# Optimization experiments

Hardware: AMD Instinct MI355X
Metric: run time of the kernel (lower is better)

## Reference

```python
import jax, jax.numpy as jnp
import numpy as np
from jax import lax

RADIUS = 8
EPS = 1e-3
EPS_LOG = 1e-6
EPS_SCALE = 1e-4
A_COMP = 0.7
B_SHIFT = 0.0
DETAIL_GAIN = 1.0
DOWN = 0.5
# detail_threshold=0 and target_mean=0 -> those branches are inactive (defaults)

DN = (('NCHW', 'OIHW', 'NCHW'))


def _box_filter(x4d):
    """Separable box filter on [1,1,H,W] with reflect padding, kernel 2r+1."""
    k = 2 * RADIUS + 1
    xp = jnp.pad(x4d, ((0, 0), (0, 0), (RADIUS, RADIUS), (RADIUS, RADIUS)), mode='reflect')
    kh = jnp.full((1, 1, 1, k), 1.0 / k, dtype=x4d.dtype)
    kv = jnp.full((1, 1, k, 1), 1.0 / k, dtype=x4d.dtype)
    y = lax.conv_general_dilated(xp, kh, (1, 1), 'VALID', dimension_numbers=DN)
    y = lax.conv_general_dilated(y, kv, (1, 1), 'VALID', dimension_numbers=DN)
    return y


def _guided_filter(img):
    """Self-guided filter on a 2D image [H, W]."""
    x4 = img[None, None]
    mean_I = _box_filter(x4)
    mean_II = _box_filter(x4 * x4)
    var_I = mean_II - mean_I * mean_I
    a = var_I / (var_I + EPS)
    b = mean_I - a * mean_I
    out = _box_filter(a) * x4 + _box_filter(b)
    return out[0, 0]


def _bilinear_resize(img, oh, ow):
    """Bilinear resize [H,W] -> [oh,ow], half-pixel centers (align_corners=False),
    no antialias, matching torch F.interpolate(mode='bilinear')."""
    H, W = img.shape
    ys = jnp.maximum((jnp.arange(oh, dtype=img.dtype) + 0.5) * (H / oh) - 0.5, 0.0)
    xs = jnp.maximum((jnp.arange(ow, dtype=img.dtype) + 0.5) * (W / ow) - 0.5, 0.0)
    y0 = jnp.floor(ys)
    x0 = jnp.floor(xs)
    wy = (ys - y0)[:, None]
    wx = (xs - x0)[None, :]
    y0i = jnp.clip(y0.astype(jnp.int32), 0, H - 1)
    y1i = jnp.minimum(y0i + 1, H - 1)
    x0i = jnp.clip(x0.astype(jnp.int32), 0, W - 1)
    x1i = jnp.minimum(x0i + 1, W - 1)
    # vertical lerp, then horizontal lerp (separable)
    vert = img[y0i, :] * (1.0 - wy) + img[y1i, :] * wy       # [oh, W]
    out = vert[:, x0i] * (1.0 - wx) + vert[:, x1i] * wx      # [oh, ow]
    return out


def setup_inputs() -> dict:
    key = jax.random.key(0)
    x = jax.random.uniform(key, (2160, 3840, 3), dtype=jnp.float32)
    return {"x": x}


def reference(x) -> jnp.ndarray:
    H, W = x.shape[0], x.shape[1]
    Y = 0.2126 * x[..., 0] + 0.7152 * x[..., 1] + 0.0722 * x[..., 2]
    Y_log = jnp.log2(jnp.maximum(Y, EPS_LOG))
    # fast path: downsample -> guided filter -> upsample
    dh, dw = int(H * DOWN), int(W * DOWN)
    Y_log_down = _bilinear_resize(Y_log, dh, dw)
    Y_base_down = _guided_filter(Y_log_down)
    Y_base = _bilinear_resize(Y_base_down, H, W)
    Y_detail = Y_log - Y_base  # detail_threshold=0 -> no suppression
    Y_tm = (A_COMP * Y_base + B_SHIFT) + DETAIL_GAIN * Y_detail
    Y_out = jnp.exp2(Y_tm)
    scale = Y_out / (Y + EPS_SCALE)
    out = jnp.clip(x * scale[..., None], 0.0, 1.0)
    # target_mean=0 -> no global mean rescale
    return out
```

## Files before the change

### kernel.cpp

```cpp
#include <hip/hip_runtime.h>
#include <math.h>

#define H_FULL 2160
#define W_FULL 3840
#define H_D    1080
#define W_D    1920
#define KLEN   17
#define INV_K2 (1.0f/289.0f)

typedef float f32x4 __attribute__((ext_vector_type(4)));

#if __has_builtin(__builtin_amdgcn_logf)
#define FAST_LOG2(x) __builtin_amdgcn_logf(x)
#else
#define FAST_LOG2(x) log2f(x)
#endif
#if __has_builtin(__builtin_amdgcn_exp2f)
#define FAST_EXP2(x) __builtin_amdgcn_exp2f(x)
#else
#define FAST_EXP2(x) exp2f(x)
#endif
#if __has_builtin(__builtin_amdgcn_rcpf)
#define FAST_RCP(x) __builtin_amdgcn_rcpf(x)
#else
#define FAST_RCP(x) (1.0f/(x))
#endif

static __device__ __forceinline__ int refl(int i, int n) {
    if (i < 0) i = -i;
    else if (i >= n) i = 2*n - 2 - i;
    return i;
}
static __device__ __forceinline__ float lum(float r, float g, float b) {
    return 0.2126f*r + 0.7152f*g + 0.0722f*b;
}
static __device__ __forceinline__ float lg(float y) {
    return FAST_LOG2(fmaxf(y, 1e-6f));
}
static __device__ __forceinline__ void nt_store4(float* p, float a, float b,
                                                 float c, float d) {
    f32x4 v; v.x = a; v.y = b; v.z = c; v.w = d;
    __builtin_nontemporal_store(v, (f32x4*)p);
}

__global__ __launch_bounds__(256) void k_down(const float* __restrict__ x,
                                              float* __restrict__ I) {
    int t = blockIdx.x * 256 + threadIdx.x;
    int p = t * 2;
    int i = p / W_D;
    int j = p - i * W_D;
    const float4* r0 = (const float4*)(x + ((size_t)(2*i)   * W_FULL + 2*j) * 3);
    const float4* r1 = (const float4*)(x + ((size_t)(2*i+1) * W_FULL + 2*j) * 3);
    float4 a0 = r0[0], a1 = r0[1], a2 = r0[2];
    float4 b0 = r1[0], b1 = r1[1], b2 = r1[2];
    float y00 = lum(a0.x,a0.y,a0.z), y01 = lum(a0.w,a1.x,a1.y);
    float y02 = lum(a1.z,a1.w,a2.x), y03 = lum(a2.y,a2.z,a2.w);
    float y10 = lum(b0.x,b0.y,b0.z), y11 = lum(b0.w,b1.x,b1.y);
    float y12 = lum(b1.z,b1.w,b2.x), y13 = lum(b2.y,b2.z,b2.w);
    float o0 = 0.25f * (lg(y00)+lg(y01)+lg(y10)+lg(y11));
    float o1 = 0.25f * (lg(y02)+lg(y03)+lg(y12)+lg(y13));
    *(float2*)(I + (size_t)i * W_D + j) = make_float2(o0, o1);
}

__global__ __launch_bounds__(512, 6) void k_fused5(const float* __restrict__ I,
                                                   const float* __restrict__ x,
                                                   float* __restrict__ out) {
    __shared__ char lds[52088];
    float*  sIc   = (float*) (lds);
    float*  sIf   = (float*) (lds + 4760);
    float2* ab    = (float2*)(lds + 4760);
    float2* hI    = (float2*)(lds + 25160);
    float2* hab   = (float2*)(lds + 25160);
    float*  baseL = (float*) (lds + 39160);
    float*  stage = (float*) (lds + 8192);

    int tx0 = blockIdx.x * 32;
    int ty0 = blockIdx.y * 32;
    int tid = threadIdx.x;

    for (int e = tid; e < 66 * 66; e += 512) {
        int r = e / 66, c = e - r * 66;
        sIf[r * 67 + c] =
            I[(size_t)refl(ty0 - 17 + r, H_D) * W_D + refl(tx0 - 17 + c, W_D)];
    }
    __syncthreads();

    if (tid < 330) {
        int r = tid / 5, run = tid - (tid / 5) * 5;
        int c0 = run * 10;
        const float* p = &sIf[r * 67 + c0];
        float s1 = 0.f, s2 = 0.f;
        #pragma unroll
        for (int k = 0; k < KLEN; ++k) { float v = p[k]; s1 += v; s2 += v * v; }
        float2* o = &hI[r * 51 + c0];
        o[0] = make_float2(s1, s2);
        #pragma unroll
        for (int m = 1; m < 10; ++m) {
            float vo = p[m - 1], vi = p[m + 16];
            s1 += vi - vo;
            s2 += vi * vi - vo * vo;
            o[m] = make_float2(s1, s2);
        }
    }
    for (int e = tid; e < 34 * 34; e += 512) {
        int r = e / 34, c = e - r * 34;
        sIc[r * 35 + c] = sIf[(r + 16) * 67 + (c + 16)];
    }
    __syncthreads();

    if (tid < 250) {
        int c = tid % 50, run = tid / 50;
        int r0 = run * 10;
        const float2* p = &hI[r0 * 51 + c];
        float s1 = 0.f, s2 = 0.f;
        #pragma unroll
        for (int k = 0; k < KLEN; ++k) { float2 v = p[k * 51]; s1 += v.x; s2 += v.y; }
        float2* o = &ab[r0 * 51 + c];
        #pragma unroll
        for (int m = 0; m < 10; ++m) {
            if (m) {
                float2 vi = p[(m + 16) * 51], vo = p[(m - 1) * 51];
                s1 += vi.x - vo.x;
                s2 += vi.y - vo.y;
            }
            float mI  = s1 * INV_K2;
            float mII = s2 * INV_K2;
            float var = mII - mI * mI;
            float av  = var / (var + 1e-3f);
            o[m * 51] = make_float2(av, mI - av * mI);
        }
    }
    __syncthreads();

    if (tid < 200) {
        int r = tid % 50, run = tid / 50;
        int c0  = (run < 2) ? run * 9 : 18 + (run - 2) * 8;
        int len = (run < 2) ? 9 : 8;
        const float2* p = &ab[r * 51 + c0];
        float sa = 0.f, sb = 0.f;
        #pragma unroll
        for (int k = 0; k < KLEN; ++k) { float2 v = p[k]; sa += v.x; sb += v.y; }
        float2* o = &hab[r * 35 + c0];
        o[0] = make_float2(sa, sb);
        #pragma unroll
        for (int m = 1; m < 9; ++m) {
            if (m < len) {
                float2 vi = p[m + 16], vo = p[m - 1];
                sa += vi.x - vo.x;
                sb += vi.y - vo.y;
                o[m] = make_float2(sa, sb);
            }
        }
    }
    __syncthreads();

    if (tid < 136) {
        int cc = tid % 34, run = tid / 34;
        int r0  = (run < 2) ? run * 9 : 18 + (run - 2) * 8;
        int len = (run < 2) ? 9 : 8;
        const float2* p = &hab[r0 * 35 + cc];
        float sa = 0.f, sb = 0.f;
        #pragma unroll
        for (int k = 0; k < KLEN; ++k) { float2 v = p[k * 35]; sa += v.x; sb += v.y; }
        #pragma unroll
        for (int m = 0; m < 9; ++m) {
            if (m < len) {
                if (m) {
                    float2 vi = p[(m + 16) * 35], vo = p[(m - 1) * 35];
                    sa += vi.x - vo.x;
                    sb += vi.y - vo.y;
                }
                int br = r0 + m;
                baseL[br * 35 + cc] =
                    (sa * INV_K2) * sIc[br * 35 + cc] + sb * INV_K2;
            }
        }
    }
    __syncthreads();

    int q  = tid & 15;
    int r  = tid >> 4;
    int gc0 = tx0 + 2 * q - 1;
    int l0 = max(gc0, 0) - (tx0 - 1);
    int l1 = 2 * q + 1, l2 = 2 * q + 2;
    int l3 = min(gc0 + 3, W_D - 1) - (tx0 - 1);
    int j0 = tx0 * 2 + q * 4;

    #pragma unroll
    for (int s = 0; s < 2; ++s) {
        int oy = ty0 * 2 + r + s * 32;
        if (oy < H_FULL) {
            int y0g = (oy - 1) >> 1;
            int ly0 = max(y0g, 0) - (ty0 - 1);
            int ly1 = min(y0g + 1, H_D - 1) - (ty0 - 1);
            float wy = (oy & 1) ? 0.25f : 0.75f;
            const float* b0r = &baseL[ly0 * 35];
            const float* b1r = &baseL[ly1 * 35];
            float v0 = b0r[l0] + (b1r[l0] - b0r[l0]) * wy;
            float v1 = b0r[l1] + (b1r[l1] - b0r[l1]) * wy;
            float v2 = b0r[l2] + (b1r[l2] - b0r[l2]) * wy;
            float v3 = b0r[l3] + (b1r[l3] - b0r[l3]) * wy;
            float Yb[4];
            Yb[0] = v0 + (v1 - v0) * 0.75f;
            Yb[1] = v1 + (v2 - v1) * 0.25f;
            Yb[2] = v1 + (v2 - v1) * 0.75f;
            Yb[3] = v2 + (v3 - v2) * 0.25f;

            size_t off = ((size_t)oy * W_FULL + j0) * 3;
            const float4* px = (const float4*)(x + off);
            float4 q0 = px[0], q1 = px[1], q2 = px[2];
            float rgb[12] = {q0.x,q0.y,q0.z,q0.w, q1.x,q1.y,q1.z,q1.w, q2.x,q2.y,q2.z,q2.w};
            float res[12];
            #pragma unroll
            for (int k = 0; k < 4; ++k) {
                float rr = rgb[3*k], gg = rgb[3*k+1], bb = rgb[3*k+2];
                float Y = lum(rr, gg, bb);
                float sc = fmaxf(Y, 1e-6f) * FAST_EXP2(-0.3f * Yb[k]) * FAST_RCP(Y + 1e-4f);
                res[3*k]   = fminf(fmaxf(rr * sc, 0.f), 1.f);
                res[3*k+1] = fminf(fmaxf(gg * sc, 0.f), 1.f);
                res[3*k+2] = fminf(fmaxf(bb * sc, 0.f), 1.f);
            }
            float* st = stage + r * 192 + q * 12;
            *(float4*)(st)     = make_float4(res[0], res[1], res[2],  res[3]);
            *(float4*)(st + 4) = make_float4(res[4], res[5], res[6],  res[7]);
            *(float4*)(st + 8) = make_float4(res[8], res[9], res[10], res[11]);
        }
        __syncthreads();

        int rowbase = ty0 * 2 + s * 32;
        #pragma unroll
        for (int k = 0; k < 3; ++k) {
            int f4 = tid + k * 512;
            int rr = f4 / 48, cc = f4 - rr * 48;
            if (rowbase + rr < H_FULL) {
                float4 v = *((float4*)stage + f4);
                float* po = out + ((size_t)(rowbase + rr) * W_FULL + tx0 * 2) * 3 + cc * 4;
                nt_store4(po, v.x, v.y, v.z, v.w);
            }
        }
        if (s == 0) __syncthreads();
    }
}

extern "C" void kernel_launch(void* const* d_in, const int* in_sizes, int n_in,
                              void* d_out, int out_size, void* d_ws, size_t ws_size,
                              hipStream_t stream) {
    (void)in_sizes; (void)n_in; (void)out_size; (void)ws_size;
    const float* x = (const float*)d_in[0];
    float* out = (float*)d_out;
    float* I = (float*)d_ws;

    k_down  <<<dim3(4050, 1, 1), dim3(256, 1, 1), 0, stream>>>(x, I);
    k_fused5<<<dim3(60, 34, 1),  dim3(512, 1, 1), 0, stream>>>(I, x, out);
}
```

Before: 67.24 us.

## Split fused filter+tonemap into separate filter and per-row tonemap kernels

Moves the upsample and tone-map stage out of the fused guided-filter kernel. The filter kernel now writes the downsampled base layer to a workspace plane, and a new streaming kernel processes 16 full-res pixels per thread with direct vectorized loads and stores. This removes the LDS staging and extra barriers from the fused kernel so the heavy full-res read and write can run at higher occupancy. In exchange it adds an extra global write and read of the base plane and one more kernel launch.

```diff
diff --git a/kernel.cpp b/kernel.cpp
--- a/kernel.cpp
+++ b/kernel.cpp
@@ -62,9 +62,8 @@
     *(float2*)(I + (size_t)i * W_D + j) = make_float2(o0, o1);
 }
 
-__global__ __launch_bounds__(512, 6) void k_fused5(const float* __restrict__ I,
-                                                   const float* __restrict__ x,
-                                                   float* __restrict__ out) {
+__global__ __launch_bounds__(512, 6) void k_filter(const float* __restrict__ I,
+                                                   float* __restrict__ base) {
     __shared__ char lds[52088];
     float*  sIc   = (float*) (lds);
     float*  sIf   = (float*) (lds + 4760);
@@ -72,7 +71,6 @@
     float2* hI    = (float2*)(lds + 25160);
     float2* hab   = (float2*)(lds + 25160);
     float*  baseL = (float*) (lds + 39160);
-    float*  stage = (float*) (lds + 8192);
 
     int tx0 = blockIdx.x * 32;
     int ty0 = blockIdx.y * 32;
@@ -178,68 +176,73 @@
     }
     __syncthreads();
 
-    int q  = tid & 15;
-    int r  = tid >> 4;
-    int gc0 = tx0 + 2 * q - 1;
-    int l0 = max(gc0, 0) - (tx0 - 1);
-    int l1 = 2 * q + 1, l2 = 2 * q + 2;
-    int l3 = min(gc0 + 3, W_D - 1) - (tx0 - 1);
-    int j0 = tx0 * 2 + q * 4;
-
-    #pragma unroll
-    for (int s = 0; s < 2; ++s) {
-        int oy = ty0 * 2 + r + s * 32;
-        if (oy < H_FULL) {
-            int y0g = (oy - 1) >> 1;
-            int ly0 = max(y0g, 0) - (ty0 - 1);
-            int ly1 = min(y0g + 1, H_D - 1) - (ty0 - 1);
-            float wy = (oy & 1) ? 0.25f : 0.75f;
-            const float* b0r = &baseL[ly0 * 35];
-            const float* b1r = &baseL[ly1 * 35];
-            float v0 = b0r[l0] + (b1r[l0] - b0r[l0]) * wy;
-            float v1 = b0r[l1] + (b1r[l1] - b0r[l1]) * wy;
-            float v2 = b0r[l2] + (b1r[l2] - b0r[l2]) * wy;
-            float v3 = b0r[l3] + (b1r[l3] - b0r[l3]) * wy;
-            float Yb[4];
-            Yb[0] = v0 + (v1 - v0) * 0.75f;
-            Yb[1] = v1 + (v2 - v1) * 0.25f;
-            Yb[2] = v1 + (v2 - v1) * 0.75f;
-            Yb[3] = v2 + (v3 - v2) * 0.25f;
-
-            size_t off = ((size_t)oy * W_FULL + j0) * 3;
-            const float4* px = (const float4*)(x + off);
-            float4 q0 = px[0], q1 = px[1], q2 = px[2];
-            float rgb[12] = {q0.x,q0.y,q0.z,q0.w, q1.x,q1.y,q1.z,q1.w, q2.x,q2.y,q2.z,q2.w};
-            float res[12];
-            #pragma unroll
-            for (int k = 0; k < 4; ++k) {
-                float rr = rgb[3*k], gg = rgb[3*k+1], bb = rgb[3*k+2];
-                float Y = lum(rr, gg, bb);
-                float sc = fmaxf(Y, 1e-6f) * FAST_EXP2(-0.3f * Yb[k]) * FAST_RCP(Y + 1e-4f);
-                res[3*k]   = fminf(fmaxf(rr * sc, 0.f), 1.f);
-                res[3*k+1] = fminf(fmaxf(gg * sc, 0.f), 1.f);
-                res[3*k+2] = fminf(fmaxf(bb * sc, 0.f), 1.f);
-            }
-            float* st = stage + r * 192 + q * 12;
-            *(float4*)(st)     = make_float4(res[0], res[1], res[2],  res[3]);
-            *(float4*)(st + 4) = make_float4(res[4], res[5], res[6],  res[7]);
-            *(float4*)(st + 8) = make_float4(res[8], res[9], res[10], res[11]);
-        }
-        __syncthreads();
-
-        int rowbase = ty0 * 2 + s * 32;
-        #pragma unroll
-        for (int k = 0; k < 3; ++k) {
-            int f4 = tid + k * 512;
-            int rr = f4 / 48, cc = f4 - rr * 48;
-            if (rowbase + rr < H_FULL) {
-                float4 v = *((float4*)stage + f4);
-                float* po = out + ((size_t)(rowbase + rr) * W_FULL + tx0 * 2) * 3 + cc * 4;
-                nt_store4(po, v.x, v.y, v.z, v.w);
-            }
-        }
-        if (s == 0) __syncthreads();
-    }
+    for (int e = tid; e < 32 * 32; e += 512) {
+        int r = e >> 5, c = e & 31;
+        int gr = ty0 + r;
+        if (gr < H_D) base[(size_t)gr * W_D + (tx0 + c)] = baseL[(r + 1) * 35 + (c + 1)];
+    }
+}
+
+__global__ __launch_bounds__(256) void k_tm16(const float* __restrict__ x,
+                                              const float* __restrict__ base,
+                                              float* __restrict__ out) {
+    int t = blockIdx.x * 256 + threadIdx.x;
+    int oy = t / 240;
+    int g  = t - oy * 240;
+    int j0 = g * 16;
+
+    int y0g = (oy - 1) >> 1;
+    int y0 = max(y0g, 0);
+    int y1 = min(y0g + 1, H_D - 1);
+    float wy = (oy & 1) ? 0.25f : 0.75f;
+    const float* b0 = base + (size_t)y0 * W_D;
+    const float* b1 = base + (size_t)y1 * W_D;
+
+    size_t off = ((size_t)oy * W_FULL + j0) * 3;
+    const float4* px = (const float4*)(x + off);
+    float4 q[12];
+    #pragma unroll
+    for (int i = 0; i < 12; ++i) q[i] = px[i];
+
+    float Yb[16];
+    #pragma unroll
+    for (int s = 0; s < 4; ++s) {
+        int k2 = g * 8 + 2 * s;
+        int c0 = max(k2 - 1, 0);
+        int c3 = min(k2 + 2, W_D - 1);
+        float u0 = b0[c0],     w0 = b1[c0];
+        float u1 = b0[k2],     w1 = b1[k2];
+        float u2 = b0[k2 + 1], w2 = b1[k2 + 1];
+        float u3 = b0[c3],     w3 = b1[c3];
+        float v0 = u0 + (w0 - u0) * wy;
+        float v1 = u1 + (w1 - u1) * wy;
+        float v2 = u2 + (w2 - u2) * wy;
+        float v3 = u3 + (w3 - u3) * wy;
+        Yb[4*s+0] = v0 + (v1 - v0) * 0.75f;
+        Yb[4*s+1] = v1 + (v2 - v1) * 0.25f;
+        Yb[4*s+2] = v1 + (v2 - v1) * 0.75f;
+        Yb[4*s+3] = v2 + (v3 - v2) * 0.25f;
+    }
+
+    float f[48];
+    #pragma unroll
+    for (int i = 0; i < 12; ++i) {
+        f[4*i] = q[i].x; f[4*i+1] = q[i].y; f[4*i+2] = q[i].z; f[4*i+3] = q[i].w;
+    }
+    float res[48];
+    #pragma unroll
+    for (int k = 0; k < 16; ++k) {
+        float rr = f[3*k], gg = f[3*k+1], bb = f[3*k+2];
+        float Y = lum(rr, gg, bb);
+        float sc = fmaxf(Y, 1e-6f) * FAST_EXP2(-0.3f * Yb[k]) * FAST_RCP(Y + 1e-4f);
+        res[3*k]   = fminf(fmaxf(rr * sc, 0.f), 1.f);
+        res[3*k+1] = fminf(fmaxf(gg * sc, 0.f), 1.f);
+        res[3*k+2] = fminf(fmaxf(bb * sc, 0.f), 1.f);
+    }
+    float* po = out + off;
+    #pragma unroll
+    for (int i = 0; i < 12; ++i)
+        nt_store4(po + 4*i, res[4*i], res[4*i+1], res[4*i+2], res[4*i+3]);
 }
 
 extern "C" void kernel_launch(void* const* d_in, const int* in_sizes, int n_in,
@@ -249,7 +252,10 @@
     const float* x = (const float*)d_in[0];
     float* out = (float*)d_out;
     float* I = (float*)d_ws;
+    size_t plane = (size_t)H_D * W_D;
+    float* base = I + plane;
 
     k_down  <<<dim3(4050, 1, 1), dim3(256, 1, 1), 0, stream>>>(x, I);
-    k_fused5<<<dim3(60, 34, 1),  dim3(512, 1, 1), 0, stream>>>(I, x, out);
-}
+    k_filter<<<dim3(60, 34, 1),  dim3(512, 1, 1), 0, stream>>>(I, base);
+    k_tm16  <<<dim3(2025, 1, 1), dim3(256, 1, 1), 0, stream>>>(x, base, out);
+}
```

After: 171.9 us. 156% more time.
